# Kernel optimization log

Hardware: AMD Instinct MI355X
Metric: run time of the kernel (lower is better)

The kernel has to match this reference:

```python
import jax, jax.numpy as jnp
import numpy as np

SIGMA = 0.02          # walker step std
CORR_LEN = 10         # correlation_length
N = 65536             # n_samples (walkers)
NE = 16               # n_elec
D = NE * 3            # flattened coord dim
H = 256               # surrogate MLP hidden


def setup_inputs() -> dict:
    key = jax.random.key(0)
    ks = jax.random.split(key, 6)
    return {
        "curr_sample": jax.random.normal(ks[0], (N, NE, 3), jnp.float32),
        "W1": jax.random.normal(ks[1], (D, H), jnp.float32) * 0.1,
        "b1": jnp.zeros((H,), jnp.float32),
        "w2": jax.random.normal(ks[2], (H,), jnp.float32) * 0.1,
        "Wh": jax.random.normal(ks[3], (D, H), jnp.float32) * 0.1,
        "bh": jnp.zeros((H,), jnp.float32),
        "wh2": jax.random.normal(ks[4], (H,), jnp.float32) * 0.1,
    }


def _log_amp(x, W, b, w):
    # x: [n, NE, 3] -> scalar log-amplitude per walker: [n]
    f = x.reshape(x.shape[0], -1)
    return jnp.tanh(f @ W + b) @ w


def reference(curr_sample, W1, b1, w2, Wh, bh, wh2):
    n = curr_sample.shape[0]
    half = n // 2
    sm = curr_sample[:half]   # model-sampled walkers
    sh = curr_sample[half:]   # HF-sampled walkers
    # to_prob(log_amp) = exp(log_amp)**2 = exp(2*log_amp)
    pm = jnp.exp(2.0 * _log_amp(sm, W1, b1, w2))
    ph = jnp.exp(2.0 * _log_amp(sh, Wh, bh, wh2))

    step_keys = jax.random.split(jax.random.key(42), CORR_LEN)

    def step(carry, k):
        sm, pm, sh, ph = carry
        k1, k2, k3, k4 = jax.random.split(k, 4)
        new_sm = sm + SIGMA * jax.random.normal(k1, sm.shape, sm.dtype)
        new_pm = jnp.exp(2.0 * _log_amp(new_sm, W1, b1, w2))
        new_sh = sh + SIGMA * jax.random.normal(k2, sh.shape, sh.dtype)
        new_ph = jnp.exp(2.0 * _log_amp(new_sh, Wh, bh, wh2))
        mm = (new_pm / pm) > jax.random.uniform(k3, (half,), sm.dtype)
        mh = (new_ph / ph) > jax.random.uniform(k4, (half,), sh.dtype)
        sm = jnp.where(mm[:, None, None], new_sm, sm)
        pm = jnp.where(mm, new_pm, pm)
        sh = jnp.where(mh[:, None, None], new_sh, sh)
        ph = jnp.where(mh, new_ph, ph)
        return (sm, pm, sh, ph), None

    (sm, pm, sh, ph), _ = jax.lax.scan(step, (sm, pm, sh, ph), step_keys)
    out = jnp.concatenate([sm, sh], axis=0)
    perm = jax.random.permutation(jax.random.key(7), n)  # torch.randperm analog
    return out[perm]
```

## Files before the change

kernel.cpp:

```cpp
#include <hip/hip_runtime.h>
#include <cstdint>
#include <cstring>
#include <vector>
#include <numeric>
#include <algorithm>


typedef __attribute__((ext_vector_type(2))) float f32x2;
typedef __attribute__((ext_vector_type(4))) float f32x4;

static constexpr int kHalfN = 32768;
static constexpr int kSteps = 10;
static constexpr int kD = 48;
static constexpr int kH = 256;
static constexpr int kS = 8;
static constexpr int kWPB = 8;
static constexpr int kXW = kD * kS;

struct StepKeys {
  uint32_t kn[2][kSteps][2];
  uint32_t ku[2][kSteps][2];
};

__host__ __device__ __forceinline__ void tf2x32(uint32_t k0, uint32_t k1,
                                                uint32_t x0, uint32_t x1,
                                                uint32_t& y0, uint32_t& y1) {
  const uint32_t ks2 = k0 ^ k1 ^ 0x1BD11BDAu;
  x0 += k0; x1 += k1;
#define TFR(r) do { x0 += x1; x1 = (x1 << (r)) | (x1 >> (32 - (r))); x1 ^= x0; } while (0)
  TFR(13); TFR(15); TFR(26); TFR(6);
  x0 += k1;  x1 += ks2 + 1u;
  TFR(17); TFR(29); TFR(16); TFR(24);
  x0 += ks2; x1 += k0 + 2u;
  TFR(13); TFR(15); TFR(26); TFR(6);
  x0 += k0;  x1 += k1 + 3u;
  TFR(17); TFR(29); TFR(16); TFR(24);
  x0 += k1;  x1 += ks2 + 4u;
  TFR(13); TFR(15); TFR(26); TFR(6);
  x0 += ks2; x1 += k0 + 5u;
#undef TFR
  y0 = x0; y1 = x1;
}

__device__ __forceinline__ uint32_t tf_xor(uint32_t k0, uint32_t k1, uint32_t i) {
  uint32_t a, b;
  tf2x32(k0, k1, 0u, i, a, b);
  return a ^ b;
}

__device__ __forceinline__ float unit_from_bits(uint32_t bits) {
  return __uint_as_float((bits >> 9) | 0x3F800000u) - 1.0f;
}

__device__ __forceinline__ float normal_from_bits(uint32_t bits) {
  const float f  = unit_from_bits(bits);
  const float lo = __uint_as_float(0xBF7FFFFFu);
  float u = __fadd_rn(__fmul_rn(f, 2.0f), lo);
  u = fmaxf(u, lo);
  const float uu = __fmul_rn(u, u);
  float w = -__logf(1.0f - uu);
  float p;
  if (w < 5.0f) {
    w = w - 2.5f;
    p = 2.81022636e-08f;
    p = fmaf(p, w, 3.43273939e-07f);
    p = fmaf(p, w, -3.5233877e-06f);
    p = fmaf(p, w, -4.39150654e-06f);
    p = fmaf(p, w, 0.00021858087f);
    p = fmaf(p, w, -0.00125372503f);
    p = fmaf(p, w, -0.00417768164f);
    p = fmaf(p, w, 0.246640727f);
    p = fmaf(p, w, 1.50140941f);
  } else {
    w = sqrtf(w) - 3.0f;
    p = -0.000200214257f;
    p = fmaf(p, w, 0.000100950558f);
    p = fmaf(p, w, 0.00134934322f);
    p = fmaf(p, w, -0.00367342844f);
    p = fmaf(p, w, 0.00573950773f);
    p = fmaf(p, w, -0.0076224613f);
    p = fmaf(p, w, 0.00943887047f);
    p = fmaf(p, w, 1.00167406f);
    p = fmaf(p, w, 2.83297682f);
  }
  return __fmul_rn(__uint_as_float(0x3FB504F3u), __fmul_rn(p, u));
}

__device__ __forceinline__ float readlane_f(float v, int l) {
  return __int_as_float(__builtin_amdgcn_readlane(__float_as_int(v), l));
}

__device__ __forceinline__ float fast_tanh(float x) {
  const float xc = fminf(x, 44.0f);
  const float t = __expf(xc + xc);
  const float a = t + 1.0f;
  float r = __builtin_amdgcn_rcpf(a);
  r = r * (2.0f - a * r);
  return fmaf(-2.0f, r, 1.0f);
}

__device__ __forceinline__ void mlpS(const float* __restrict__ sW,
                                     const float* __restrict__ sX,
                                     int lane,
                                     const float breg[4], const float wreg[4],
                                     float p[kS]) {
  f32x2 acc[4][4];
#pragma unroll
  for (int sp = 0; sp < 4; ++sp)
#pragma unroll
    for (int m = 0; m < 4; ++m) acc[sp][m] = (f32x2){0.f, 0.f};
  const float* wp = sW + (lane << 2);
#pragma unroll 4
  for (int d = 0; d < kD; ++d) {
    const f32x4 w4 = *reinterpret_cast<const f32x4*>(wp + (d << 8));
    const f32x2 w01 = __builtin_shufflevector(w4, w4, 0, 1);
    const f32x2 w23 = __builtin_shufflevector(w4, w4, 2, 3);
    const float* xr = sX + (d << 3);
    const f32x4 xa = *reinterpret_cast<const f32x4*>(xr);
    const f32x4 xb = *reinterpret_cast<const f32x4*>(xr + 4);
    f32x2 f2[4];
    f2[0] = __builtin_shufflevector(xa, xa, 0, 1);
    f2[1] = __builtin_shufflevector(xa, xa, 2, 3);
    f2[2] = __builtin_shufflevector(xb, xb, 0, 1);
    f2[3] = __builtin_shufflevector(xb, xb, 2, 3);
#pragma unroll
    for (int sp = 0; sp < 4; ++sp) {
      asm("v_pk_fma_f32 %0, %1, %2, %0 op_sel_hi:[0,1,1]"
          : "+v"(acc[sp][0]) : "v"(w01), "v"(f2[sp]));
      asm("v_pk_fma_f32 %0, %1, %2, %0 op_sel:[1,0,0] op_sel_hi:[1,1,1]"
          : "+v"(acc[sp][1]) : "v"(w01), "v"(f2[sp]));
      asm("v_pk_fma_f32 %0, %1, %2, %0 op_sel_hi:[0,1,1]"
          : "+v"(acc[sp][2]) : "v"(w23), "v"(f2[sp]));
      asm("v_pk_fma_f32 %0, %1, %2, %0 op_sel:[1,0,0] op_sel_hi:[1,1,1]"
          : "+v"(acc[sp][3]) : "v"(w23), "v"(f2[sp]));
    }
  }
#pragma unroll
  for (int s = 0; s < kS; ++s) {
    const int sp = s >> 1, h = s & 1;
    float pv = 0.f;
#pragma unroll
    for (int m = 0; m < 4; ++m)
      pv = fmaf(fast_tanh(acc[sp][m][h] + breg[m]), wreg[m], pv);
#pragma unroll
    for (int o = 1; o < 64; o <<= 1) pv += __shfl_xor(pv, o);
    p[s] = pv;
  }
}

__device__ __forceinline__ void writeX(float* __restrict__ sX, int lane,
                                       const float v[kS]) {
  if (lane < kD) {
    float* xr = sX + (lane << 3);
#pragma unroll
    for (int sp = 0; sp < 4; ++sp) {
      f32x2 t = {v[2 * sp], v[2 * sp + 1]};
      *reinterpret_cast<f32x2*>(xr + 2 * sp) = t;
    }
  }
}

__global__ __launch_bounds__(512, 4) void mh_chain_kernel(
    const float* __restrict__ curr,
    const float* __restrict__ W1, const float* __restrict__ b1, const float* __restrict__ w2,
    const float* __restrict__ Wh, const float* __restrict__ bh, const float* __restrict__ wh2,
    const uint32_t* __restrict__ iperm,
    float* __restrict__ out,
    StepKeys keys)
{
  __shared__ float sW[kD * kH];
  __shared__ float sX[kWPB * kXW];
  const int bid  = (int)blockIdx.x;
  const int half = bid >> 9;
  const float* W    = half ? Wh  : W1;
  const float* bsrc = half ? bh  : b1;
  const float* wsrc = half ? wh2 : w2;

  for (int j = (int)threadIdx.x; j < kD * kH; j += 512) {
    const int d = j >> 8, cc = j & 255;
    sW[j] = W[(d << 8) | ((cc >> 2) | ((cc & 3) << 6))];
  }
  __syncthreads();

  const int wv   = (int)(threadIdx.x >> 6);
  const int lane = (int)(threadIdx.x & 63);
  float* xw = sX + wv * kXW;
  const int base    = ((bid & 511) << 6) | (wv << 3);
  const int rowBase = half * kHalfN + base;

  float breg[4], wreg[4];
#pragma unroll
  for (int m = 0; m < 4; ++m) {
    breg[m] = bsrc[lane + 64 * m];
    wreg[m] = wsrc[lane + 64 * m];
  }

  float sv[kS];
#pragma unroll
  for (int s = 0; s < kS; ++s)
    sv[s] = (lane < kD) ? curr[(rowBase + s) * kD + lane] : 0.f;

  writeX(xw, lane, sv);
  float p0[kS];
  mlpS(sW, xw, lane, breg, wreg, p0);
  float pc[kS];
#pragma unroll
  for (int s = 0; s < kS; ++s) pc[s] = __expf(__fmul_rn(2.0f, p0[s]));

#pragma unroll 1
  for (int t = 0; t < kSteps; ++t) {
    const uint32_t kn0 = keys.kn[half][t][0], kn1 = keys.kn[half][t][1];
    const uint32_t ku0 = keys.ku[half][t][0], ku1 = keys.ku[half][t][1];

    float u[kS], nw[kS];
    {
      const bool noiser = lane < kD;
      const uint32_t k0 = noiser ? kn0 : ku0;
      const uint32_t k1 = noiser ? kn1 : ku1;
      const uint32_t ctr = noiser ? (uint32_t)(base * kD + lane)
                                  : (uint32_t)(base + lane - 48);
      const uint32_t bits = tf_xor(k0, k1, ctr);
      const float nv = normal_from_bits(bits);
      const float uvv = unit_from_bits(bits);
#pragma unroll
      for (int s = 0; s < kS; ++s) u[s] = readlane_f(uvv, 48 + s);
      nw[0] = __fadd_rn(sv[0], __fmul_rn(0.02f, nv));
    }
#pragma unroll
    for (int s = 1; s < kS; ++s) {
      const uint32_t bits = tf_xor(kn0, kn1, (uint32_t)((base + s) * kD + lane));
      nw[s] = __fadd_rn(sv[s], __fmul_rn(0.02f, normal_from_bits(bits)));
    }

    writeX(xw, lane, nw);
    float pn[kS];
    mlpS(sW, xw, lane, breg, wreg, pn);
#pragma unroll
    for (int s = 0; s < kS; ++s) {
      const float e = __expf(__fmul_rn(2.0f, pn[s]));
      const bool ok = __fdiv_rn(e, pc[s]) > u[s];
      sv[s] = ok ? nw[s] : sv[s];
      pc[s] = ok ? e : pc[s];
    }
  }

#pragma unroll
  for (int s = 0; s < kS; ++s) {
    const int dst = (int)iperm[rowBase + s];
    if (lane < kD) out[dst * kD + lane] = sv[s];
  }
}

struct HostInit {
  StepKeys keys;
  uint32_t iperm[65536];
  HostInit() {
    const uint32_t k42_0 = 0u, k42_1 = 42u;
    for (int t = 0; t < kSteps; ++t) {
      uint32_t sk0, sk1;
      tf2x32(k42_0, k42_1, 0u, (uint32_t)t, sk0, sk1);
      uint32_t k[4][2];
      for (int j = 0; j < 4; ++j) tf2x32(sk0, sk1, 0u, (uint32_t)j, k[j][0], k[j][1]);
      keys.kn[0][t][0] = k[0][0]; keys.kn[0][t][1] = k[0][1];
      keys.kn[1][t][0] = k[1][0]; keys.kn[1][t][1] = k[1][1];
      keys.ku[0][t][0] = k[2][0]; keys.ku[0][t][1] = k[2][1];
      keys.ku[1][t][0] = k[3][0]; keys.ku[1][t][1] = k[3][1];
    }
    const int n = 65536;
    uint32_t kc0 = 0u, kc1 = 7u;
    std::vector<uint32_t> bits(n), val(n), idx(n), nv(n);
    std::iota(val.begin(), val.end(), 0u);
    for (int r = 0; r < 2; ++r) {
      uint32_t nk0, nk1, sub0, sub1;
      tf2x32(kc0, kc1, 0u, 0u, nk0, nk1);
      tf2x32(kc0, kc1, 0u, 1u, sub0, sub1);
      kc0 = nk0; kc1 = nk1;
      for (int i = 0; i < n; ++i) {
        uint32_t a, b;
        tf2x32(sub0, sub1, 0u, (uint32_t)i, a, b);
        bits[i] = a ^ b;
      }
      std::iota(idx.begin(), idx.end(), 0u);
      std::stable_sort(idx.begin(), idx.end(),
                       [&](uint32_t x, uint32_t y) { return bits[x] < bits[y]; });
      for (int i = 0; i < n; ++i) nv[i] = val[idx[i]];
      val.swap(nv);
    }
    for (int i = 0; i < n; ++i) iperm[val[i]] = (uint32_t)i;
  }
};
static const HostInit g_init;

extern "C" void kernel_launch(void* const* d_in, const int* in_sizes, int n_in,
                              void* d_out, int out_size, void* d_ws, size_t ws_size,
                              hipStream_t stream) {
  (void)in_sizes; (void)n_in; (void)out_size; (void)ws_size;
  const float* curr = (const float*)d_in[0];
  const float* W1   = (const float*)d_in[1];
  const float* b1   = (const float*)d_in[2];
  const float* w2   = (const float*)d_in[3];
  const float* Wh   = (const float*)d_in[4];
  const float* bh   = (const float*)d_in[5];
  const float* wh2  = (const float*)d_in[6];
  float* out = (float*)d_out;

  hipMemcpyAsync(d_ws, g_init.iperm, sizeof(g_init.iperm),
                 hipMemcpyHostToDevice, stream);

  mh_chain_kernel<<<dim3(1024), dim3(512), 0, stream>>>(
      curr, W1, b1, w2, Wh, bh, wh2, (const uint32_t*)d_ws, out, g_init.keys);
}
```

Baseline: 455.9 us.

## Use swizzle reductions, warp-uniform erfinv branch, division-free accept, relaxed launch bounds

The normal-from-bits routine now always evaluates the central polynomial and runs the tail branch only if some lane needs it, which removes per-lane divergence. The 64-lane butterfly reduction in the MLP switches from __shfl_xor to ds_swizzle steps for offsets up to 16. The acceptance test compares e > u*pc instead of doing a correctly rounded division, and the uniform readlanes move into the accept loop to cut register use. Launch bounds go from 4 to 2 blocks per CU, giving more registers at the cost of occupancy. The multiply-compare can round differently from the original divide, so a few borderline accept decisions may flip.

```diff
diff --git a/kernel.cpp b/kernel.cpp
--- a/kernel.cpp
+++ b/kernel.cpp
@@ -59,29 +59,28 @@
   u = fmaxf(u, lo);
   const float uu = __fmul_rn(u, u);
   float w = -__logf(1.0f - uu);
-  float p;
-  if (w < 5.0f) {
-    w = w - 2.5f;
-    p = 2.81022636e-08f;
-    p = fmaf(p, w, 3.43273939e-07f);
-    p = fmaf(p, w, -3.5233877e-06f);
-    p = fmaf(p, w, -4.39150654e-06f);
-    p = fmaf(p, w, 0.00021858087f);
-    p = fmaf(p, w, -0.00125372503f);
-    p = fmaf(p, w, -0.00417768164f);
-    p = fmaf(p, w, 0.246640727f);
-    p = fmaf(p, w, 1.50140941f);
-  } else {
-    w = sqrtf(w) - 3.0f;
-    p = -0.000200214257f;
-    p = fmaf(p, w, 0.000100950558f);
-    p = fmaf(p, w, 0.00134934322f);
-    p = fmaf(p, w, -0.00367342844f);
-    p = fmaf(p, w, 0.00573950773f);
-    p = fmaf(p, w, -0.0076224613f);
-    p = fmaf(p, w, 0.00943887047f);
-    p = fmaf(p, w, 1.00167406f);
-    p = fmaf(p, w, 2.83297682f);
+  float wc = w - 2.5f;
+  float p = 2.81022636e-08f;
+  p = fmaf(p, wc, 3.43273939e-07f);
+  p = fmaf(p, wc, -3.5233877e-06f);
+  p = fmaf(p, wc, -4.39150654e-06f);
+  p = fmaf(p, wc, 0.00021858087f);
+  p = fmaf(p, wc, -0.00125372503f);
+  p = fmaf(p, wc, -0.00417768164f);
+  p = fmaf(p, wc, 0.246640727f);
+  p = fmaf(p, wc, 1.50140941f);
+  if (__any(w >= 5.0f)) {
+    float wt = sqrtf(w) - 3.0f;
+    float q = -0.000200214257f;
+    q = fmaf(q, wt, 0.000100950558f);
+    q = fmaf(q, wt, 0.00134934322f);
+    q = fmaf(q, wt, -0.00367342844f);
+    q = fmaf(q, wt, 0.00573950773f);
+    q = fmaf(q, wt, -0.0076224613f);
+    q = fmaf(q, wt, 0.00943887047f);
+    q = fmaf(q, wt, 1.00167406f);
+    q = fmaf(q, wt, 2.83297682f);
+    p = (w < 5.0f) ? p : q;
   }
   return __fmul_rn(__uint_as_float(0x3FB504F3u), __fmul_rn(p, u));
 }
@@ -97,6 +96,16 @@
   float r = __builtin_amdgcn_rcpf(a);
   r = r * (2.0f - a * r);
   return fmaf(-2.0f, r, 1.0f);
+}
+
+__device__ __forceinline__ float wave_sum64(float v) {
+  v += __int_as_float(__builtin_amdgcn_ds_swizzle(__float_as_int(v), 0x041F));
+  v += __int_as_float(__builtin_amdgcn_ds_swizzle(__float_as_int(v), 0x081F));
+  v += __int_as_float(__builtin_amdgcn_ds_swizzle(__float_as_int(v), 0x101F));
+  v += __int_as_float(__builtin_amdgcn_ds_swizzle(__float_as_int(v), 0x201F));
+  v += __int_as_float(__builtin_amdgcn_ds_swizzle(__float_as_int(v), 0x401F));
+  v += __shfl_xor(v, 32);
+  return v;
 }
 
 __device__ __forceinline__ void mlpS(const float* __restrict__ sW,
@@ -142,9 +151,7 @@
 #pragma unroll
     for (int m = 0; m < 4; ++m)
       pv = fmaf(fast_tanh(acc[sp][m][h] + breg[m]), wreg[m], pv);
-#pragma unroll
-    for (int o = 1; o < 64; o <<= 1) pv += __shfl_xor(pv, o);
-    p[s] = pv;
+    p[s] = wave_sum64(pv);
   }
 }
 
@@ -160,7 +167,7 @@
   }
 }
 
-__global__ __launch_bounds__(512, 4) void mh_chain_kernel(
+__global__ __launch_bounds__(512, 2) void mh_chain_kernel(
     const float* __restrict__ curr,
     const float* __restrict__ W1, const float* __restrict__ b1, const float* __restrict__ w2,
     const float* __restrict__ Wh, const float* __restrict__ bh, const float* __restrict__ wh2,
@@ -212,7 +219,7 @@
     const uint32_t kn0 = keys.kn[half][t][0], kn1 = keys.kn[half][t][1];
     const uint32_t ku0 = keys.ku[half][t][0], ku1 = keys.ku[half][t][1];
 
-    float u[kS], nw[kS];
+    float uvv, nw[kS];
     {
       const bool noiser = lane < kD;
       const uint32_t k0 = noiser ? kn0 : ku0;
@@ -221,9 +228,7 @@
                                   : (uint32_t)(base + lane - 48);
       const uint32_t bits = tf_xor(k0, k1, ctr);
       const float nv = normal_from_bits(bits);
-      const float uvv = unit_from_bits(bits);
-#pragma unroll
-      for (int s = 0; s < kS; ++s) u[s] = readlane_f(uvv, 48 + s);
+      uvv = unit_from_bits(bits);
       nw[0] = __fadd_rn(sv[0], __fmul_rn(0.02f, nv));
     }
 #pragma unroll
@@ -238,7 +243,8 @@
 #pragma unroll
     for (int s = 0; s < kS; ++s) {
       const float e = __expf(__fmul_rn(2.0f, pn[s]));
-      const bool ok = __fdiv_rn(e, pc[s]) > u[s];
+      const float us = readlane_f(uvv, 48 + s);
+      const bool ok = e > __fmul_rn(us, pc[s]);
       sv[s] = ok ? nw[s] : sv[s];
       pc[s] = ok ? e : pc[s];
     }
```

New measurement: 427.0 us. -6.3%, faster.
